# Optimization experiments

Hardware: AMD Instinct MI355X
Metric: run time of the kernel (lower is better)

## Reference

```python
import jax, jax.numpy as jnp
import numpy as np

B, S, E, H = 2, 2048, 1024, 16
D = E // H  # head_dim = 64


def setup_inputs() -> dict:
    key = jax.random.key(0)
    ks = jax.random.split(key, 6)
    scale = 1.0 / np.sqrt(E)
    x = jax.random.normal(ks[0], (B, S, E), dtype=jnp.float32)
    mask = jnp.ones((B, S), dtype=jnp.int32)
    Wqkv = jax.random.normal(ks[1], (E, 3 * E), dtype=jnp.float32) * scale
    bqkv = jax.random.normal(ks[2], (3 * E,), dtype=jnp.float32) * 0.01
    Wout = jax.random.normal(ks[3], (E, E), dtype=jnp.float32) * scale
    bout = jax.random.normal(ks[4], (E,), dtype=jnp.float32) * 0.01
    return {"x": x, "mask": mask, "Wqkv": Wqkv, "bqkv": bqkv, "Wout": Wout, "bout": bout}


def reference(x, mask, Wqkv, bqkv, Wout, bout):
    Bn, Sn, En = x.shape
    qkv = x @ Wqkv + bqkv                      # [B,S,3E]
    qkv = qkv.reshape(Bn, Sn, 3, H, D)
    qkv = jnp.transpose(qkv, (2, 0, 3, 1, 4))  # [3,B,H,S,D]
    q, k, v = qkv[0], qkv[1], qkv[2]
    scores = jnp.einsum('bhqd,bhkd->bhqk', q, k) / np.sqrt(D).astype(np.float32)
    m = mask[:, None, None, :]                 # [B,1,1,S]
    scores = jnp.where(m == 0, jnp.float32(-jnp.inf), scores)
    attn = jax.nn.softmax(scores, axis=-1)
    out = jnp.einsum('bhqk,bhkd->bhqd', attn, v)  # [B,H,S,D]
    out = jnp.transpose(out, (0, 2, 1, 3)).reshape(Bn, Sn, En)
    return out @ Wout + bout
```

## Files before the change

kernel.cpp:

```cpp
#include <hip/hip_runtime.h>


typedef __attribute__((ext_vector_type(8))) short short8;
typedef __attribute__((ext_vector_type(4))) float floatx4;
typedef unsigned short ushort_t;

static __device__ __forceinline__ ushort_t f2bf(float f) {
    unsigned u = __float_as_uint(f);
    u += 0x7fffu + ((u >> 16) & 1u);
    return (ushort_t)(u >> 16);
}
static __device__ __forceinline__ float bf2f(ushort_t h) {
    return __uint_as_float(((unsigned)h) << 16);
}
static __device__ __forceinline__ float hexp2(float x) {
    return __builtin_amdgcn_exp2f(x);
}
static __device__ __forceinline__ void gload16(const void* g, void* l) {
    __builtin_amdgcn_global_load_lds(
        (const __attribute__((address_space(1))) unsigned int*)g,
        (__attribute__((address_space(3))) unsigned int*)l, 16, 0, 0);
}

__global__ __launch_bounds__(256) void conv_split(const float* __restrict__ in,
                                                  ushort_t* __restrict__ hi,
                                                  ushort_t* __restrict__ lo) {
    int i = blockIdx.x * 256 + threadIdx.x;
    float4 v = ((const float4*)in)[i];
    ushort_t hh[4], ll[4];
    hh[0] = f2bf(v.x); hh[1] = f2bf(v.y); hh[2] = f2bf(v.z); hh[3] = f2bf(v.w);
    ll[0] = f2bf(v.x - bf2f(hh[0])); ll[1] = f2bf(v.y - bf2f(hh[1]));
    ll[2] = f2bf(v.z - bf2f(hh[2])); ll[3] = f2bf(v.w - bf2f(hh[3]));
    ((uint2*)hi)[i] = *(const uint2*)hh;
    ((uint2*)lo)[i] = *(const uint2*)ll;
}

__global__ __launch_bounds__(256) void conv_T_hi(const float* __restrict__ W,
                                                 ushort_t* __restrict__ hiT,
                                                 int K, int N) {
    __shared__ float tile[32][33];
    const int nb = blockIdx.x * 32, kb = blockIdx.y * 32;
    const int t = threadIdx.x;
    const int r = t >> 3, c4 = (t & 7) * 4;
    float4 v = *(const float4*)&W[(size_t)(kb + r) * N + nb + c4];
    tile[r][c4 + 0] = v.x; tile[r][c4 + 1] = v.y;
    tile[r][c4 + 2] = v.z; tile[r][c4 + 3] = v.w;
    __syncthreads();
    ushort_t hh[4];
    #pragma unroll
    for (int j = 0; j < 4; ++j) hh[j] = f2bf(tile[c4 + j][r]);
    size_t o = ((size_t)(nb + r) * K + kb + c4) >> 2;
    ((uint2*)hiT)[o] = *(const uint2*)hh;
}

__global__ __launch_bounds__(256) void transpose_v(const ushort_t* __restrict__ qkvb,
                                                   ushort_t* __restrict__ vtg) {
    __shared__ ushort_t tile[64][72];
    const int b = blockIdx.z, h = blockIdx.y, s0 = blockIdx.x * 64;
    const int t = threadIdx.x;
    #pragma unroll
    for (int p = 0; p < 2; ++p) {
        int idx = t + p * 256;
        int sl = idx >> 3, dc = (idx & 7) * 8;
        *(uint4*)&tile[sl][dc] =
            *(const uint4*)&qkvb[(size_t)(b * 2048 + s0 + sl) * 3072 + 2048 + h * 64 + dc];
    }
    __syncthreads();
    #pragma unroll
    for (int p = 0; p < 2; ++p) {
        int idx = t + p * 256;
        int dl = idx >> 3, sc = (idx & 7) * 8;
        ushort_t v[8];
        #pragma unroll
        for (int j = 0; j < 8; ++j) v[j] = tile[sc + j][dl];
        *(uint4*)&vtg[(size_t)((b * 16 + h) * 64 + dl) * 2048 + s0 + sc] = *(const uint4*)v;
    }
}

__global__ __launch_bounds__(256, 3) void gemm_split2(
    const ushort_t* __restrict__ Ahi, const ushort_t* __restrict__ Alo,
    const ushort_t* __restrict__ Bhi,
    const float* __restrict__ bias, ushort_t* __restrict__ C,
    int M, int N, int K)
{
    __shared__ ushort_t Ah[128][32], Al[128][32], Bh[128][32];
    const int bn = blockIdx.x * 128, bm = blockIdx.y * 128;
    const int t = threadIdx.x, w = t >> 6, lane = t & 63;
    const int l15 = lane & 15, quad = lane >> 4;
    const int wm = w >> 1, wn = w & 1;

    const int srow = w * 32 + (lane >> 2);
    const int skp  = (lane & 3) ^ ((lane >> 2) & 3);
    const int scol = skp * 8;
    const ushort_t* ga  = Ahi + (size_t)(bm + srow) * K + scol;
    const ushort_t* gal = Alo + (size_t)(bm + srow) * K + scol;
    const ushort_t* gb  = Bhi + (size_t)(bn + srow) * K + scol;
    const size_t rstep = (size_t)16 * K;

    const int fcol = ((quad ^ (l15 & 3)) * 8);

    floatx4 acc[4][4];
    #pragma unroll
    for (int mt = 0; mt < 4; ++mt)
        #pragma unroll
        for (int nt = 0; nt < 4; ++nt) acc[mt][nt] = (floatx4){0.f, 0.f, 0.f, 0.f};

    for (int k0 = 0; k0 < K; k0 += 32) {
        #pragma unroll
        for (int i = 0; i < 2; ++i) {
            gload16(ga  + i * rstep + k0, &Ah[w * 32 + i * 16][0]);
            gload16(gal + i * rstep + k0, &Al[w * 32 + i * 16][0]);
            gload16(gb  + i * rstep + k0, &Bh[w * 32 + i * 16][0]);
        }
        __syncthreads();
        short8 ah[4], al[4], bh[4];
        #pragma unroll
        for (int x = 0; x < 4; ++x) {
            ah[x] = *(const short8*)&Ah[wm * 64 + x * 16 + l15][fcol];
            al[x] = *(const short8*)&Al[wm * 64 + x * 16 + l15][fcol];
            bh[x] = *(const short8*)&Bh[wn * 64 + x * 16 + l15][fcol];
        }
        #pragma unroll
        for (int mt = 0; mt < 4; ++mt)
            #pragma unroll
            for (int nt = 0; nt < 4; ++nt) {
                acc[mt][nt] = __builtin_amdgcn_mfma_f32_16x16x32_bf16(ah[mt], bh[nt], acc[mt][nt], 0, 0, 0);
                acc[mt][nt] = __builtin_amdgcn_mfma_f32_16x16x32_bf16(al[mt], bh[nt], acc[mt][nt], 0, 0, 0);
            }
        __syncthreads();
    }
    #pragma unroll
    for (int mt = 0; mt < 4; ++mt)
        #pragma unroll
        for (int r = 0; r < 4; ++r) {
            size_t row = (size_t)(bm + wm * 64 + mt * 16 + quad * 4 + r) * N;
            #pragma unroll
            for (int nt = 0; nt < 4; ++nt) {
                int col = bn + wn * 64 + nt * 16 + l15;
                C[row + col] = f2bf(acc[mt][nt][r] + bias[col]);
            }
        }
}

__global__ __launch_bounds__(256, 3) void gemm_bf16(
    const ushort_t* __restrict__ A, const ushort_t* __restrict__ B,
    const float* __restrict__ bias, float* __restrict__ C,
    int M, int N, int K)
{
    __shared__ ushort_t Ah[128][32], Bh[128][32];
    const int bn = blockIdx.x * 128, bm = blockIdx.y * 128;
    const int t = threadIdx.x, w = t >> 6, lane = t & 63;
    const int l15 = lane & 15, quad = lane >> 4;
    const int wm = w >> 1, wn = w & 1;

    const int srow = w * 32 + (lane >> 2);
    const int skp  = (lane & 3) ^ ((lane >> 2) & 3);
    const int scol = skp * 8;
    const ushort_t* ga = A + (size_t)(bm + srow) * K + scol;
    const ushort_t* gb = B + (size_t)(bn + srow) * K + scol;
    const size_t rstep = (size_t)16 * K;
    const int fcol = ((quad ^ (l15 & 3)) * 8);

    floatx4 acc[4][4];
    #pragma unroll
    for (int mt = 0; mt < 4; ++mt)
        #pragma unroll
        for (int nt = 0; nt < 4; ++nt) acc[mt][nt] = (floatx4){0.f, 0.f, 0.f, 0.f};

    for (int k0 = 0; k0 < K; k0 += 32) {
        #pragma unroll
        for (int i = 0; i < 2; ++i) {
            gload16(ga + i * rstep + k0, &Ah[w * 32 + i * 16][0]);
            gload16(gb + i * rstep + k0, &Bh[w * 32 + i * 16][0]);
        }
        __syncthreads();
        short8 ah[4], bh[4];
        #pragma unroll
        for (int x = 0; x < 4; ++x) {
            ah[x] = *(const short8*)&Ah[wm * 64 + x * 16 + l15][fcol];
            bh[x] = *(const short8*)&Bh[wn * 64 + x * 16 + l15][fcol];
        }
        #pragma unroll
        for (int mt = 0; mt < 4; ++mt)
            #pragma unroll
            for (int nt = 0; nt < 4; ++nt)
                acc[mt][nt] = __builtin_amdgcn_mfma_f32_16x16x32_bf16(ah[mt], bh[nt], acc[mt][nt], 0, 0, 0);
        __syncthreads();
    }
    #pragma unroll
    for (int mt = 0; mt < 4; ++mt)
        #pragma unroll
        for (int r = 0; r < 4; ++r) {
            size_t row = (size_t)(bm + wm * 64 + mt * 16 + quad * 4 + r) * N;
            #pragma unroll
            for (int nt = 0; nt < 4; ++nt) {
                int col = bn + wn * 64 + nt * 16 + l15;
                C[row + col] = acc[mt][nt][r] + bias[col];
            }
        }
}

__global__ __launch_bounds__(256, 2) void flash_v3(
    const ushort_t* __restrict__ qkv, const ushort_t* __restrict__ vtg,
    const int* __restrict__ mask, ushort_t* __restrict__ attn, int S)
{
    __shared__ ushort_t Ks[64][64];
    __shared__ ushort_t Vt[64][64];
    __shared__ ushort_t Ps[4][16][72];
    __shared__ float Madd[64];

    const int b = blockIdx.z, h = blockIdx.y, q0 = blockIdx.x * 128;
    const int t = threadIdx.x, wave = t >> 6, lane = t & 63;
    const int l15 = lane & 15, quad = lane >> 4;
    const size_t bS = (size_t)b * S;
    const float c1  = 0.125f * 1.44269504088896340736f;
    const float OFF = 24.0f;

    short8 qf[2][2];
    #pragma unroll
    for (int tt = 0; tt < 2; ++tt) {
        int q = q0 + wave * 32 + tt * 16 + l15;
        const ushort_t* qp = qkv + (bS + q) * 3072 + h * 64;
        qf[tt][0] = *(const short8*)(qp + quad * 8);
        qf[tt][1] = *(const short8*)(qp + 32 + quad * 8);
    }

    const int srow  = wave * 16 + (lane >> 3);
    const int schnk = ((lane & 7) ^ ((lane >> 3) & 7)) * 8;
    const ushort_t* gK = qkv + (bS + srow) * 3072 + 1024 + h * 64 + schnk;
    const ushort_t* gV = vtg + ((size_t)(b * 16 + h) * 64 + srow) * 2048 + schnk;

    floatx4 outacc[2][4];
    float lsum[2] = {0.f, 0.f};
    #pragma unroll
    for (int tt = 0; tt < 2; ++tt)
        #pragma unroll
        for (int dt = 0; dt < 4; ++dt) outacc[tt][dt] = (floatx4){0.f, 0.f, 0.f, 0.f};

    for (int k0 = 0; k0 < S; k0 += 64) {
        gload16(gK + (size_t)k0 * 3072,              &Ks[wave * 16][0]);
        gload16(gK + (size_t)k0 * 3072 + 8 * 3072,   &Ks[wave * 16 + 8][0]);
        gload16(gV + k0,                             &Vt[wave * 16][0]);
        gload16(gV + k0 + 8 * 2048,                  &Vt[wave * 16 + 8][0]);
        if (t < 64) Madd[t] = (mask[bS + k0 + t] ? 0.f : -1e30f) - OFF;
        __syncthreads();

        short8 kf[2][4], vf[2][4];
        #pragma unroll
        for (int kc = 0; kc < 2; ++kc)
            #pragma unroll
            for (int c = 0; c < 4; ++c) {
                int ch = ((kc * 4 + quad) ^ (l15 & 7)) * 8;
                kf[kc][c] = *(const short8*)&Ks[c * 16 + l15][ch];
                vf[kc][c] = *(const short8*)&Vt[c * 16 + l15][ch];
            }
        float4 madd4[4];
        #pragma unroll
        for (int c = 0; c < 4; ++c) madd4[c] = *(const float4*)&Madd[c * 16 + quad * 4];

        #pragma unroll
        for (int tt = 0; tt < 2; ++tt) {
            floatx4 sc[4];
            #pragma unroll
            for (int c = 0; c < 4; ++c) {
                sc[c] = (floatx4){0.f, 0.f, 0.f, 0.f};
                sc[c] = __builtin_amdgcn_mfma_f32_16x16x32_bf16(kf[0][c], qf[tt][0], sc[c], 0, 0, 0);
                sc[c] = __builtin_amdgcn_mfma_f32_16x16x32_bf16(kf[1][c], qf[tt][1], sc[c], 0, 0, 0);
            }
            #pragma unroll
            for (int c = 0; c < 4; ++c) {
                float p0 = hexp2(fmaf(sc[c][0], c1, madd4[c].x));
                float p1 = hexp2(fmaf(sc[c][1], c1, madd4[c].y));
                float p2 = hexp2(fmaf(sc[c][2], c1, madd4[c].z));
                float p3 = hexp2(fmaf(sc[c][3], c1, madd4[c].w));
                lsum[tt] += (p0 + p1) + (p2 + p3);
                uint2 pk;
                pk.x = (unsigned)f2bf(p0) | ((unsigned)f2bf(p1) << 16);
                pk.y = (unsigned)f2bf(p2) | ((unsigned)f2bf(p3) << 16);
                *(uint2*)&Ps[wave][l15][c * 16 + quad * 4] = pk;
            }
            short8 pf0 = *(const short8*)&Ps[wave][l15][quad * 8];
            short8 pf1 = *(const short8*)&Ps[wave][l15][32 + quad * 8];
            #pragma unroll
            for (int dt = 0; dt < 4; ++dt) {
                outacc[tt][dt] = __builtin_amdgcn_mfma_f32_16x16x32_bf16(vf[0][dt], pf0, outacc[tt][dt], 0, 0, 0);
                outacc[tt][dt] = __builtin_amdgcn_mfma_f32_16x16x32_bf16(vf[1][dt], pf1, outacc[tt][dt], 0, 0, 0);
            }
        }
        __syncthreads();
    }

    #pragma unroll
    for (int tt = 0; tt < 2; ++tt) {
        lsum[tt] += __shfl_xor(lsum[tt], 16);
        lsum[tt] += __shfl_xor(lsum[tt], 32);
    }

    #pragma unroll
    for (int tt = 0; tt < 2; ++tt) {
        float inv = 1.f / lsum[tt];
        int q = q0 + wave * 32 + tt * 16 + l15;
        ushort_t* orow = attn + (bS + q) * 1024 + h * 64;
        #pragma unroll
        for (int dt = 0; dt < 4; ++dt) {
            uint2 pk;
            pk.x = (unsigned)f2bf(outacc[tt][dt][0] * inv) |
                   ((unsigned)f2bf(outacc[tt][dt][1] * inv) << 16);
            pk.y = (unsigned)f2bf(outacc[tt][dt][2] * inv) |
                   ((unsigned)f2bf(outacc[tt][dt][3] * inv) << 16);
            *(uint2*)&orow[dt * 16 + quad * 4] = pk;
        }
    }
}

extern "C" void kernel_launch(void* const* d_in, const int* in_sizes, int n_in,
                              void* d_out, int out_size, void* d_ws, size_t ws_size,
                              hipStream_t stream) {
    const float* x    = (const float*)d_in[0];
    const int*   mask = (const int*)  d_in[1];
    const float* Wqkv = (const float*)d_in[2];
    const float* bqkv = (const float*)d_in[3];
    const float* Wout = (const float*)d_in[4];
    const float* bout = (const float*)d_in[5];
    float* out = (float*)d_out;

    char* ws = (char*)d_ws;
    ushort_t* xhi  = (ushort_t*)(ws);
    ushort_t* xlo  = (ushort_t*)(ws + 8388608);
    ushort_t* wqT  = (ushort_t*)(ws + 16777216);
    ushort_t* qkvb = (ushort_t*)(ws + 23068672);
    ushort_t* attnb= (ushort_t*)(ws + 48234496);
    ushort_t* woT  = (ushort_t*)(ws + 56623104);
    ushort_t* vtg  = (ushort_t*)(ws + 58720256);

    const int M = 4096, E = 1024, N3 = 3072, S = 2048;

    conv_split<<<dim3(M * E / 1024), dim3(256), 0, stream>>>(x, xhi, xlo);
    conv_T_hi<<<dim3(N3 / 32, E / 32), dim3(256), 0, stream>>>(Wqkv, wqT, E, N3);

    gemm_split2<<<dim3(N3 / 128, M / 128), dim3(256), 0, stream>>>(
        xhi, xlo, wqT, bqkv, qkvb, M, N3, E);

    transpose_v<<<dim3(S / 64, 16, 2), dim3(256), 0, stream>>>(qkvb, vtg);

    flash_v3<<<dim3(S / 128, 16, 2), dim3(256), 0, stream>>>(qkvb, vtg, mask, attnb, S);

    conv_T_hi<<<dim3(E / 32, E / 32), dim3(256), 0, stream>>>(Wout, woT, E, E);

    gemm_bf16<<<dim3(E / 128, M / 128), dim3(256), 0, stream>>>(
        attnb, woT, bout, out, M, E, E);
}
```

Before: 229.5 us.

## Drop split-bf16 QKV GEMM, retile flash attention with XCD-aware grid, use packed bf16 cvt

```diff
diff --git a/kernel.cpp b/kernel.cpp
--- a/kernel.cpp
+++ b/kernel.cpp
@@ -10,9 +10,17 @@
     u += 0x7fffu + ((u >> 16) & 1u);
     return (ushort_t)(u >> 16);
 }
-static __device__ __forceinline__ float bf2f(ushort_t h) {
-    return __uint_as_float(((unsigned)h) << 16);
-}
+#if __has_builtin(__builtin_amdgcn_cvt_pk_bf16_f32)
+typedef __attribute__((ext_vector_type(2))) __bf16 bf16x2_t;
+static __device__ __forceinline__ unsigned pack2bf(float a, float b) {
+    bf16x2_t r = __builtin_amdgcn_cvt_pk_bf16_f32(a, b);
+    return __builtin_bit_cast(unsigned, r);
+}
+#else
+static __device__ __forceinline__ unsigned pack2bf(float a, float b) {
+    return (unsigned)f2bf(a) | ((unsigned)f2bf(b) << 16);
+}
+#endif
 static __device__ __forceinline__ float hexp2(float x) {
     return __builtin_amdgcn_exp2f(x);
 }
@@ -22,17 +30,14 @@
         (__attribute__((address_space(3))) unsigned int*)l, 16, 0, 0);
 }
 
-__global__ __launch_bounds__(256) void conv_split(const float* __restrict__ in,
-                                                  ushort_t* __restrict__ hi,
-                                                  ushort_t* __restrict__ lo) {
+__global__ __launch_bounds__(256) void conv_hi(const float* __restrict__ in,
+                                               ushort_t* __restrict__ out) {
     int i = blockIdx.x * 256 + threadIdx.x;
     float4 v = ((const float4*)in)[i];
-    ushort_t hh[4], ll[4];
-    hh[0] = f2bf(v.x); hh[1] = f2bf(v.y); hh[2] = f2bf(v.z); hh[3] = f2bf(v.w);
-    ll[0] = f2bf(v.x - bf2f(hh[0])); ll[1] = f2bf(v.y - bf2f(hh[1]));
-    ll[2] = f2bf(v.z - bf2f(hh[2])); ll[3] = f2bf(v.w - bf2f(hh[3]));
-    ((uint2*)hi)[i] = *(const uint2*)hh;
-    ((uint2*)lo)[i] = *(const uint2*)ll;
+    uint2 o;
+    o.x = pack2bf(v.x, v.y);
+    o.y = pack2bf(v.z, v.w);
+    ((uint2*)out)[i] = o;
 }
 
 __global__ __launch_bounds__(256) void conv_T_hi(const float* __restrict__ W,
@@ -46,11 +51,11 @@
     tile[r][c4 + 0] = v.x; tile[r][c4 + 1] = v.y;
     tile[r][c4 + 2] = v.z; tile[r][c4 + 3] = v.w;
     __syncthreads();
-    ushort_t hh[4];
-    #pragma unroll
-    for (int j = 0; j < 4; ++j) hh[j] = f2bf(tile[c4 + j][r]);
-    size_t o = ((size_t)(nb + r) * K + kb + c4) >> 2;
-    ((uint2*)hiT)[o] = *(const uint2*)hh;
+    uint2 o;
+    o.x = pack2bf(tile[c4 + 0][r], tile[c4 + 1][r]);
+    o.y = pack2bf(tile[c4 + 2][r], tile[c4 + 3][r]);
+    size_t off = ((size_t)(nb + r) * K + kb + c4) >> 2;
+    ((uint2*)hiT)[off] = o;
 }
 
 __global__ __launch_bounds__(256) void transpose_v(const ushort_t* __restrict__ qkvb,
@@ -77,13 +82,12 @@
     }
 }
 
-__global__ __launch_bounds__(256, 3) void gemm_split2(
-    const ushort_t* __restrict__ Ahi, const ushort_t* __restrict__ Alo,
-    const ushort_t* __restrict__ Bhi,
+__global__ __launch_bounds__(256, 3) void gemm_bf16_bf(
+    const ushort_t* __restrict__ A, const ushort_t* __restrict__ B,
     const float* __restrict__ bias, ushort_t* __restrict__ C,
     int M, int N, int K)
 {
-    __shared__ ushort_t Ah[128][32], Al[128][32], Bh[128][32];
+    __shared__ ushort_t Ah[128][32], Bh[128][32];
     const int bn = blockIdx.x * 128, bm = blockIdx.y * 128;
     const int t = threadIdx.x, w = t >> 6, lane = t & 63;
     const int l15 = lane & 15, quad = lane >> 4;
@@ -92,11 +96,9 @@
     const int srow = w * 32 + (lane >> 2);
     const int skp  = (lane & 3) ^ ((lane >> 2) & 3);
     const int scol = skp * 8;
-    const ushort_t* ga  = Ahi + (size_t)(bm + srow) * K + scol;
-    const ushort_t* gal = Alo + (size_t)(bm + srow) * K + scol;
-    const ushort_t* gb  = Bhi + (size_t)(bn + srow) * K + scol;
+    const ushort_t* ga = A + (size_t)(bm + srow) * K + scol;
+    const ushort_t* gb = B + (size_t)(bn + srow) * K + scol;
     const size_t rstep = (size_t)16 * K;
-
     const int fcol = ((quad ^ (l15 & 3)) * 8);
 
     floatx4 acc[4][4];
@@ -108,25 +110,21 @@
     for (int k0 = 0; k0 < K; k0 += 32) {
         #pragma unroll
         for (int i = 0; i < 2; ++i) {
-            gload16(ga  + i * rstep + k0, &Ah[w * 32 + i * 16][0]);
-            gload16(gal + i * rstep + k0, &Al[w * 32 + i * 16][0]);
-            gload16(gb  + i * rstep + k0, &Bh[w * 32 + i * 16][0]);
-        }
-        __syncthreads();
-        short8 ah[4], al[4], bh[4];
+            gload16(ga + i * rstep + k0, &Ah[w * 32 + i * 16][0]);
+            gload16(gb + i * rstep + k0, &Bh[w * 32 + i * 16][0]);
+        }
+        __syncthreads();
+        short8 ah[4], bh[4];
         #pragma unroll
         for (int x = 0; x < 4; ++x) {
             ah[x] = *(const short8*)&Ah[wm * 64 + x * 16 + l15][fcol];
-            al[x] = *(const short8*)&Al[wm * 64 + x * 16 + l15][fcol];
             bh[x] = *(const short8*)&Bh[wn * 64 + x * 16 + l15][fcol];
         }
         #pragma unroll
         for (int mt = 0; mt < 4; ++mt)
             #pragma unroll
-            for (int nt = 0; nt < 4; ++nt) {
+            for (int nt = 0; nt < 4; ++nt)
                 acc[mt][nt] = __builtin_amdgcn_mfma_f32_16x16x32_bf16(ah[mt], bh[nt], acc[mt][nt], 0, 0, 0);
-                acc[mt][nt] = __builtin_amdgcn_mfma_f32_16x16x32_bf16(al[mt], bh[nt], acc[mt][nt], 0, 0, 0);
-            }
         __syncthreads();
     }
     #pragma unroll
@@ -142,7 +140,7 @@
         }
 }
 
-__global__ __launch_bounds__(256, 3) void gemm_bf16(
+__global__ __launch_bounds__(256, 3) void gemm_bf16_f32(
     const ushort_t* __restrict__ A, const ushort_t* __restrict__ B,
     const float* __restrict__ bias, float* __restrict__ C,
     int M, int N, int K)
@@ -200,7 +198,7 @@
         }
 }
 
-__global__ __launch_bounds__(256, 2) void flash_v3(
+__global__ __launch_bounds__(256, 4) void flash_v4(
     const ushort_t* __restrict__ qkv, const ushort_t* __restrict__ vtg,
     const int* __restrict__ mask, ushort_t* __restrict__ attn, int S)
 {
@@ -209,20 +207,23 @@
     __shared__ ushort_t Ps[4][16][72];
     __shared__ float Madd[64];
 
-    const int b = blockIdx.z, h = blockIdx.y, q0 = blockIdx.x * 128;
+    const int blk = blockIdx.x;
+    const int xcd = blk & 7, rr = blk >> 3;
+    const int qi = rr & 31, gg = xcd + 8 * (rr >> 5);
+    const int b = gg >> 4, h = gg & 15, q0 = qi * 64;
+
     const int t = threadIdx.x, wave = t >> 6, lane = t & 63;
     const int l15 = lane & 15, quad = lane >> 4;
     const size_t bS = (size_t)b * S;
     const float c1  = 0.125f * 1.44269504088896340736f;
     const float OFF = 24.0f;
 
-    short8 qf[2][2];
-    #pragma unroll
-    for (int tt = 0; tt < 2; ++tt) {
-        int q = q0 + wave * 32 + tt * 16 + l15;
+    short8 qf[2];
+    {
+        int q = q0 + wave * 16 + l15;
         const ushort_t* qp = qkv + (bS + q) * 3072 + h * 64;
-        qf[tt][0] = *(const short8*)(qp + quad * 8);
-        qf[tt][1] = *(const short8*)(qp + 32 + quad * 8);
+        qf[0] = *(const short8*)(qp + quad * 8);
+        qf[1] = *(const short8*)(qp + 32 + quad * 8);
     }
 
     const int srow  = wave * 16 + (lane >> 3);
@@ -230,18 +231,16 @@
     const ushort_t* gK = qkv + (bS + srow) * 3072 + 1024 + h * 64 + schnk;
     const ushort_t* gV = vtg + ((size_t)(b * 16 + h) * 64 + srow) * 2048 + schnk;
 
-    floatx4 outacc[2][4];
-    float lsum[2] = {0.f, 0.f};
-    #pragma unroll
-    for (int tt = 0; tt < 2; ++tt)
-        #pragma unroll
-        for (int dt = 0; dt < 4; ++dt) outacc[tt][dt] = (floatx4){0.f, 0.f, 0.f, 0.f};
+    floatx4 outacc[4];
+    float lsum = 0.f;
+    #pragma unroll
+    for (int dt = 0; dt < 4; ++dt) outacc[dt] = (floatx4){0.f, 0.f, 0.f, 0.f};
 
     for (int k0 = 0; k0 < S; k0 += 64) {
-        gload16(gK + (size_t)k0 * 3072,              &Ks[wave * 16][0]);
-        gload16(gK + (size_t)k0 * 3072 + 8 * 3072,   &Ks[wave * 16 + 8][0]);
-        gload16(gV + k0,                             &Vt[wave * 16][0]);
-        gload16(gV + k0 + 8 * 2048,                  &Vt[wave * 16 + 8][0]);
+        gload16(gK + (size_t)k0 * 3072,             &Ks[wave * 16][0]);
+        gload16(gK + (size_t)k0 * 3072 + 8 * 3072,  &Ks[wave * 16 + 8][0]);
+        gload16(gV + k0,                            &Vt[wave * 16][0]);
+        gload16(gV + k0 + 8 * 2048,                 &Vt[wave * 16 + 8][0]);
         if (t < 64) Madd[t] = (mask[bS + k0 + t] ? 0.f : -1e30f) - OFF;
         __syncthreads();
 
@@ -258,56 +257,47 @@
         #pragma unroll
         for (int c = 0; c < 4; ++c) madd4[c] = *(const float4*)&Madd[c * 16 + quad * 4];
 
-        #pragma unroll
-        for (int tt = 0; tt < 2; ++tt) {
-            floatx4 sc[4];
-            #pragma unroll
-            for (int c = 0; c < 4; ++c) {
-                sc[c] = (floatx4){0.f, 0.f, 0.f, 0.f};
-                sc[c] = __builtin_amdgcn_mfma_f32_16x16x32_bf16(kf[0][c], qf[tt][0], sc[c], 0, 0, 0);
-                sc[c] = __builtin_amdgcn_mfma_f32_16x16x32_bf16(kf[1][c], qf[tt][1], sc[c], 0, 0, 0);
-            }
-            #pragma unroll
-            for (int c = 0; c < 4; ++c) {
-                float p0 = hexp2(fmaf(sc[c][0], c1, madd4[c].x));
-                float p1 = hexp2(fmaf(sc[c][1], c1, madd4[c].y));
-                float p2 = hexp2(fmaf(sc[c][2], c1, madd4[c].z));
-                float p3 = hexp2(fmaf(sc[c][3], c1, madd4[c].w));
-                lsum[tt] += (p0 + p1) + (p2 + p3);
-                uint2 pk;
-                pk.x = (unsigned)f2bf(p0) | ((unsigned)f2bf(p1) << 16);
-                pk.y = (unsigned)f2bf(p2) | ((unsigned)f2bf(p3) << 16);
-                *(uint2*)&Ps[wave][l15][c * 16 + quad * 4] = pk;
-            }
-            short8 pf0 = *(const short8*)&Ps[wave][l15][quad * 8];
-            short8 pf1 = *(const short8*)&Ps[wave][l15][32 + quad * 8];
-            #pragma unroll
-            for (int dt = 0; dt < 4; ++dt) {
-                outacc[tt][dt] = __builtin_amdgcn_mfma_f32_16x16x32_bf16(vf[0][dt], pf0, outacc[tt][dt], 0, 0, 0);
-                outacc[tt][dt] = __builtin_amdgcn_mfma_f32_16x16x32_bf16(vf[1][dt], pf1, outacc[tt][dt], 0, 0, 0);
-            }
-        }
-        __syncthreads();
-    }
-
-    #pragma unroll
-    for (int tt = 0; tt < 2; ++tt) {
-        lsum[tt] += __shfl_xor(lsum[tt], 16);
-        lsum[tt] += __shfl_xor(lsum[tt], 32);
-    }
-
-    #pragma unroll
-    for (int tt = 0; tt < 2; ++tt) {
-        float inv = 1.f / lsum[tt];
-        int q = q0 + wave * 32 + tt * 16 + l15;
+        floatx4 sc[4];
+        #pragma unroll
+        for (int c = 0; c < 4; ++c) {
+            sc[c] = (floatx4){0.f, 0.f, 0.f, 0.f};
+            sc[c] = __builtin_amdgcn_mfma_f32_16x16x32_bf16(kf[0][c], qf[0], sc[c], 0, 0, 0);
+            sc[c] = __builtin_amdgcn_mfma_f32_16x16x32_bf16(kf[1][c], qf[1], sc[c], 0, 0, 0);
+        }
+        #pragma unroll
+        for (int c = 0; c < 4; ++c) {
+            float p0 = hexp2(fmaf(sc[c][0], c1, madd4[c].x));
+            float p1 = hexp2(fmaf(sc[c][1], c1, madd4[c].y));
+            float p2 = hexp2(fmaf(sc[c][2], c1, madd4[c].z));
+            float p3 = hexp2(fmaf(sc[c][3], c1, madd4[c].w));
+            lsum += (p0 + p1) + (p2 + p3);
+            uint2 pk;
+            pk.x = pack2bf(p0, p1);
+            pk.y = pack2bf(p2, p3);
+            *(uint2*)&Ps[wave][l15][c * 16 + quad * 4] = pk;
+        }
+        short8 pf0 = *(const short8*)&Ps[wave][l15][quad * 8];
+        short8 pf1 = *(const short8*)&Ps[wave][l15][32 + quad * 8];
+        #pragma unroll
+        for (int dt = 0; dt < 4; ++dt) {
+            outacc[dt] = __builtin_amdgcn_mfma_f32_16x16x32_bf16(vf[0][dt], pf0, outacc[dt], 0, 0, 0);
+            outacc[dt] = __builtin_amdgcn_mfma_f32_16x16x32_bf16(vf[1][dt], pf1, outacc[dt], 0, 0, 0);
+        }
+        __syncthreads();
+    }
+
+    lsum += __shfl_xor(lsum, 16);
+    lsum += __shfl_xor(lsum, 32);
+
+    {
+        float inv = 1.f / lsum;
+        int q = q0 + wave * 16 + l15;
         ushort_t* orow = attn + (bS + q) * 1024 + h * 64;
         #pragma unroll
         for (int dt = 0; dt < 4; ++dt) {
             uint2 pk;
-            pk.x = (unsigned)f2bf(outacc[tt][dt][0] * inv) |
-                   ((unsigned)f2bf(outacc[tt][dt][1] * inv) << 16);
-            pk.y = (unsigned)f2bf(outacc[tt][dt][2] * inv) |
-                   ((unsigned)f2bf(outacc[tt][dt][3] * inv) << 16);
+            pk.x = pack2bf(outacc[dt][0] * inv, outacc[dt][1] * inv);
+            pk.y = pack2bf(outacc[dt][2] * inv, outacc[dt][3] * inv);
             *(uint2*)&orow[dt * 16 + quad * 4] = pk;
         }
     }
@@ -325,28 +315,27 @@
     float* out = (float*)d_out;
 
     char* ws = (char*)d_ws;
-    ushort_t* xhi  = (ushort_t*)(ws);
-    ushort_t* xlo  = (ushort_t*)(ws + 8388608);
-    ushort_t* wqT  = (ushort_t*)(ws + 16777216);
-    ushort_t* qkvb = (ushort_t*)(ws + 23068672);
-    ushort_t* attnb= (ushort_t*)(ws + 48234496);
-    ushort_t* woT  = (ushort_t*)(ws + 56623104);
-    ushort_t* vtg  = (ushort_t*)(ws + 58720256);
+    ushort_t* xb   = (ushort_t*)(ws);
+    ushort_t* wqT  = (ushort_t*)(ws + 8388608);
+    ushort_t* qkvb = (ushort_t*)(ws + 14680064);
+    ushort_t* attnb= (ushort_t*)(ws + 39845888);
+    ushort_t* woT  = (ushort_t*)(ws + 48234496);
+    ushort_t* vtg  = (ushort_t*)(ws + 50331648);
 
     const int M = 4096, E = 1024, N3 = 3072, S = 2048;
 
-    conv_split<<<dim3(M * E / 1024), dim3(256), 0, stream>>>(x, xhi, xlo);
+    conv_hi<<<dim3(M * E / 1024), dim3(256), 0, stream>>>(x, xb);
     conv_T_hi<<<dim3(N3 / 32, E / 32), dim3(256), 0, stream>>>(Wqkv, wqT, E, N3);
 
-    gemm_split2<<<dim3(N3 / 128, M / 128), dim3(256), 0, stream>>>(
-        xhi, xlo, wqT, bqkv, qkvb, M, N3, E);
+    gemm_bf16_bf<<<dim3(N3 / 128, M / 128), dim3(256), 0, stream>>>(
+        xb, wqT, bqkv, qkvb, M, N3, E);
 
     transpose_v<<<dim3(S / 64, 16, 2), dim3(256), 0, stream>>>(qkvb, vtg);
 
-    flash_v3<<<dim3(S / 128, 16, 2), dim3(256), 0, stream>>>(qkvb, vtg, mask, attnb, S);
+    flash_v4<<<dim3(1024), dim3(256), 0, stream>>>(qkvb, vtg, mask, attnb, S);
 
     conv_T_hi<<<dim3(E / 32, E / 32), dim3(256), 0, stream>>>(Wout, woT, E, E);
 
-    gemm_bf16<<<dim3(E / 128, M / 128), dim3(256), 0, stream>>>(
+    gemm_bf16_f32<<<dim3(E / 128, M / 128), dim3(256), 0, stream>>>(
         attnb, woT, bout, out, M, E, E);
 }
```

Result: faster. 210.3 us (-8.4%).
